# Performance work log

Measured on AMD Instinct MI355X. Metric: run time of the kernel, lower is better.

Reference implementation:

```python
import jax, jax.numpy as jnp
import numpy as np

R = 45        # num_dep_rels
L = 384       # sent_len
D = 512       # word representation dim = in_size*2
E_REL = 15    # dep_rel_emb_size
IN4 = 1024    # in_size*4
HOPS = 3
THRESH = 1e-06


def setup_inputs() -> dict:
    key = jax.random.key(0)
    ks = jax.random.split(key, 10)
    energy = jax.random.uniform(ks[0], (1, R, L, L), dtype=jnp.float32)
    word_h = jax.random.normal(ks[1], (1, L, D), dtype=jnp.float32)
    e1 = jax.random.normal(ks[2], (D,), dtype=jnp.float32)
    e2 = jax.random.normal(ks[3], (D,), dtype=jnp.float32)
    # learned params
    rel_embs = jax.random.normal(ks[4], (R, E_REL), dtype=jnp.float32)
    Wc = jax.random.normal(ks[5], (2 * D + E_REL, D), dtype=jnp.float32) * 0.02
    bc = jnp.zeros((D,), dtype=jnp.float32)
    Wk = jax.random.normal(ks[6], (HOPS, IN4, IN4), dtype=jnp.float32) * 0.02
    bk = jnp.zeros((HOPS, IN4), dtype=jnp.float32)
    Wh = jax.random.normal(ks[7], (HOPS, IN4, IN4), dtype=jnp.float32) * 0.02
    bh = jnp.zeros((HOPS, IN4), dtype=jnp.float32)
    return {"energy": energy, "word_h": word_h, "e1": e1, "e2": e2,
            "sent_len": L, "rel_embs": rel_embs, "Wc": Wc, "bc": bc,
            "Wk": Wk, "bk": bk, "Wh": Wh, "bh": bh}


def reference(energy, word_h, e1, e2, sent_len, rel_embs, Wc, bc, Wk, bk, Wh, bh):
    Ls = sent_len
    E = energy[0, :, :Ls, :Ls]                 # [R, L, L]
    marg = E.sum(axis=0)                       # [L, L] marginal energy
    # threshold back-off (try t, t/10, t/100 until some arc survives)
    m0 = marg > THRESH
    m1 = marg > THRESH * 0.1
    m2 = marg > THRESH * 0.01
    mask = jnp.where(m0.any(), m0, jnp.where(m1.any(), m1, m2))  # [L, L]

    H = word_h[0, :Ls]                         # [L, D]
    w = marg.reshape(-1)                       # [L*L] arc weights
    # rel embedding per arc: sum_r E[r,h,d] * rel_embs[r,e]
    rels = jnp.einsum('rhd,re->hde', E, rel_embs).reshape(Ls * Ls, E_REL)
    head_t = jnp.repeat(H, Ls, axis=0) * w[:, None]   # [L*L, D]
    dep_t = jnp.tile(H, (Ls, 1)) * w[:, None]         # [L*L, D]
    arc_in = jnp.concatenate([head_t, rels, dep_t], axis=1)  # [L*L, 2D+15]
    mem_bank = jax.nn.leaky_relu(arc_in @ Wc + bc)    # [L*L, D] (dropout=eval)
    maskf = mask.reshape(-1)                          # [L*L]

    # multi-hop memory attention; filtered-out arcs get zero attention weight
    inputs = jnp.concatenate([e1, e2])                # [1024]
    for i in range(HOPS):
        kv = inputs @ Wk[i] + bk[i]                   # [1024]
        k_, v_ = jnp.split(kv, 2)                     # chunk along dim 0
        k_ = jnp.tanh(k_)
        v_ = jax.nn.leaky_relu(v_)
        scores = jnp.where(maskf, mem_bank @ k_, -1e30)  # [L*L]
        dist = jax.nn.softmax(scores)
        mem_rep = dist @ mem_bank                     # [D]
        inputs = jax.nn.leaky_relu(jnp.concatenate([v_, mem_rep]) @ Wh[i] + bh[i])
    return inputs
```

## Files before the change

### kernel.cpp

```cpp
#include <hip/hip_runtime.h>
#include <hip/hip_bf16.h>
#include <cstdint>
#include <cstddef>

#define LL      147456
#define NBLK    768
#define CHB     12
#define NPACK   288

typedef __attribute__((ext_vector_type(8))) short  short8;
typedef __attribute__((ext_vector_type(4))) float  f32x4;

#define EPACK_OFF   0u
#define MARG_OFF    14155776u
#define A_OFF       14745600u
#define BT_OFF      15532032u
#define UTGP_OFF    16318464u
#define XIN_OFF     16367696u
#define KBUF_OFF    16371792u
#define VBUF_OFF    16373840u
#define PM_OFF      16379984u
#define PL_OFF      16383056u
#define PACC_OFF    16386128u
#define SRAW_OFF    17958992u
#define BLKF_OFF    18548816u

#define SKIP_LD     30.0f

static __device__ __forceinline__ ushort f2bf(float x) {
  uint u = __float_as_uint(x);
  return (ushort)((u + 0x7fffu + ((u >> 16) & 1u)) >> 16);
}
static __device__ __forceinline__ float lrelu(float x) { return fmaxf(x, 0.01f * x); }

__global__ __launch_bounds__(256) void k_prep(
    const float* __restrict__ E, uint4* __restrict__ ep,
    float* __restrict__ marg, int* __restrict__ blkflags,
    const float* __restrict__ H, const float* __restrict__ Wc,
    const float* __restrict__ rel, const float* __restrict__ bc,
    float* __restrict__ A, float* __restrict__ Btp, uint4* __restrict__ Utgp) {
  __shared__ float Hs[4][512];
  __shared__ float Ps[4][512];
  __shared__ int fsh;
  int b = blockIdx.x, t = threadIdx.x;
  if (b < 192) {
    bool roleA = (b < 96);
    int g0 = (roleA ? b : b - 96) * 4;
    const float* Wcp = Wc + (size_t)(roleA ? 0 : 527) * 512;
    float* dst = roleA ? A : Btp;
    for (int i = t; i < 4 * 512; i += 256) Hs[i >> 9][i & 511] = H[(size_t)g0 * 512 + i];
    __syncthreads();
    int cq = t & 127, q = t >> 7;
    int c0 = cq * 4;
    f32x4 acc[4];
#pragma unroll
    for (int i = 0; i < 4; ++i) acc[i] = (f32x4){0.f, 0.f, 0.f, 0.f};
    for (int k = q * 256; k < q * 256 + 256; ++k) {
      f32x4 wv = *(const f32x4*)&Wcp[(size_t)k * 512 + c0];
#pragma unroll
      for (int i = 0; i < 4; ++i) { float hv = Hs[i][k]; acc[i] += hv * wv; }
    }
    if (q == 1) {
#pragma unroll
      for (int i = 0; i < 4; ++i) *(f32x4*)&Ps[i][c0] = acc[i];
    }
    __syncthreads();
    if (q == 0) {
#pragma unroll
      for (int i = 0; i < 4; ++i) {
        acc[i] += *(const f32x4*)&Ps[i][c0];
        *(f32x4*)&dst[(size_t)(g0 + i) * 512 + c0] = acc[i];
      }
    }
  } else if (b == 192) {
    for (int c = t; c < 512; c += 256) {
      float uv[48];
#pragma unroll
      for (int k = 0; k < 45; ++k) {
        float s = 0.f;
#pragma unroll
        for (int e = 0; e < 15; ++e) s += rel[k * 15 + e] * Wc[(size_t)(512 + e) * 512 + c];
        uv[k] = s;
      }
      uv[45] = bc[c]; uv[46] = 0.f; uv[47] = 0.f;
#pragma unroll
      for (int g = 0; g < 6; ++g) {
        uint w[4];
#pragma unroll
        for (int p = 0; p < 4; ++p)
          w[p] = (uint)f2bf(uv[g * 8 + 2 * p]) | ((uint)f2bf(uv[g * 8 + 2 * p + 1]) << 16);
        uint4 v; v.x = w[0]; v.y = w[1]; v.z = w[2]; v.w = w[3];
        Utgp[g * 512 + c] = v;
      }
    }
  } else {
    if (t == 0) fsh = 0;
    int bp = b - 193;
    size_t hd0 = (size_t)bp * 512 + 2 * t;
    float2 ev[46];
#pragma unroll
    for (int r = 0; r < 45; ++r) ev[r] = *(const float2*)&E[(size_t)r * LL + hd0];
    ev[45] = make_float2(1.0f, 1.0f);
    float s0 = 0.f, s1 = 0.f;
#pragma unroll
    for (int r = 0; r < 45; ++r) { s0 += ev[r].x; s1 += ev[r].y; }
#pragma unroll
    for (int o = 0; o < 6; ++o) {
      uint wa[4], wb[4];
#pragma unroll
      for (int p = 0; p < 4; ++p) {
        int r0 = 8 * o + 2 * p, r1 = r0 + 1;
        float a0 = (r0 < 46) ? ev[r0].x : 0.f, a1 = (r1 < 46) ? ev[r1].x : 0.f;
        float b0 = (r0 < 46) ? ev[r0].y : 0.f, b1 = (r1 < 46) ? ev[r1].y : 0.f;
        wa[p] = (uint)f2bf(a0) | ((uint)f2bf(a1) << 16);
        wb[p] = (uint)f2bf(b0) | ((uint)f2bf(b1) << 16);
      }
      uint4 va; va.x = wa[0]; va.y = wa[1]; va.z = wa[2]; va.w = wa[3];
      uint4 vb; vb.x = wb[0]; vb.y = wb[1]; vb.z = wb[2]; vb.w = wb[3];
      ep[(size_t)o * LL + hd0] = va;
      ep[(size_t)o * LL + hd0 + 1] = vb;
    }
    *(float2*)&marg[hd0] = make_float2(s0, s1);
    int f = (s0 > 1e-6f ? 1 : 0) | (s0 > 1e-7f ? 2 : 0) | (s0 > 1e-8f ? 4 : 0)
          | (s1 > 1e-6f ? 1 : 0) | (s1 > 1e-7f ? 2 : 0) | (s1 > 1e-8f ? 4 : 0);
#pragma unroll
    for (int d = 1; d < 64; d <<= 1) f |= __shfl_xor(f, d);
    __syncthreads();
    if ((t & 63) == 0) atomicOr(&fsh, f);
    __syncthreads();
    if (t == 0) blkflags[bp] = fsh;
  }
}

__global__ __launch_bounds__(256) void k_gemv(const float* __restrict__ W, const float* __restrict__ bias,
                                              const float* __restrict__ xA, const float* __restrict__ xB,
                                              float* __restrict__ outA, float* __restrict__ outB) {
  __shared__ float xs[1024];
  __shared__ float red[8][32];
  int t = threadIdx.x;
  for (int i = t; i < 1024; i += 256) xs[i] = (i < 512) ? xA[i] : xB[i - 512];
  __syncthreads();
  int jj = t & 31, kq = t >> 5;
  int j = blockIdx.x * 32 + jj;
  float acc = 0.f;
#pragma unroll 8
  for (int k = kq * 128; k < kq * 128 + 128; ++k) acc = fmaf(xs[k], W[(size_t)k * 1024 + j], acc);
  red[kq][jj] = acc;
  __syncthreads();
  if (kq == 0) {
    float s = bias[j];
#pragma unroll
    for (int q = 0; q < 8; ++q) s += red[q][jj];
    if (j < 512) outA[j] = tanhf(s);
    else outB[j - 512] = lrelu(s);
  }
}

__global__ __launch_bounds__(256, 3) void k_scores(
    const uint4* __restrict__ ep, const float* __restrict__ marg,
    const float* __restrict__ A, const float* __restrict__ Btp,
    const uint4* __restrict__ Utgp, const int* __restrict__ blkflags,
    const float* __restrict__ kvec,
    float* __restrict__ pm, float* __restrict__ pl, float* __restrict__ sraw) {
  __shared__ __align__(16) uint4 uthF[6 * 512];
  __shared__ float sbuf[CHB * 16];
  __shared__ float redw[8];
  __shared__ int fsh;
  int t = threadIdx.x, b = blockIdx.x;
  int dbt = b >> 5, hg = b & 31;
  int dbase = dbt * 16, h0 = hg * CHB;
  int lane = t & 63, wid = t >> 6;
  int l15 = lane & 15, qq = lane >> 4;

  if (t == 0) fsh = 0;
  for (int i = t; i < 6 * 512; i += 256) uthF[i] = Utgp[i];
  int f = 0;
  for (int i = t; i < NPACK; i += 256) f |= blkflags[i];
#pragma unroll
  for (int d = 1; d < 64; d <<= 1) f |= __shfl_xor(f, d);

  const short8 zero8 = (short8){0, 0, 0, 0, 0, 0, 0, 0};
  short8 a0[3], a1[3];
  f32x4 wq[3];
#pragma unroll
  for (int k3 = 0; k3 < 3; ++k3) {
    int h = h0 + wid * 3 + k3;
    int hda = h * 384 + dbase + l15;
    uint4 r0 = ep[(size_t)qq * LL + hda];
    a0[k3] = *(short8*)&r0;
    if (qq < 2) { uint4 r1 = ep[(size_t)(4 + qq) * LL + hda]; a1[k3] = *(short8*)&r1; }
    else a1[k3] = zero8;
    wq[k3] = *(const f32x4*)&marg[h * 384 + dbase + qq * 4];
  }
  __syncthreads();
  if ((t & 63) == 0) atomicOr(&fsh, f);

  float sp[3][4];
#pragma unroll
  for (int k3 = 0; k3 < 3; ++k3)
#pragma unroll
    for (int j = 0; j < 4; ++j) sp[k3][j] = 0.f;

  for (int half = 0; half < 2; ++half) {
    float kreg[16];
#pragma unroll
    for (int tt = 0; tt < 16; ++tt) kreg[tt] = kvec[half * 256 + tt * 16 + l15];
#pragma unroll 4
    for (int tt = 0; tt < 16; ++tt) {
      int c = half * 256 + tt * 16 + l15;
      short8 b0 = *(short8*)&uthF[qq * 512 + c];
      short8 b1 = (qq < 2) ? *(short8*)&uthF[(4 + qq) * 512 + c] : zero8;
      const float* Bp = &Btp[(size_t)(dbase + qq * 4) * 512 + c];
      float bt0 = Bp[0], bt1 = Bp[512], bt2 = Bp[1024], bt3 = Bp[1536];
      const float* Ap = &A[(size_t)(h0 + wid * 3) * 512 + c];
      float av[3]; av[0] = Ap[0]; av[1] = Ap[512]; av[2] = Ap[1024];
#pragma unroll
      for (int k3 = 0; k3 < 3; ++k3) {
        f32x4 cc = (f32x4){0.f, 0.f, 0.f, 0.f};
        cc = __builtin_amdgcn_mfma_f32_16x16x32_bf16(a0[k3], b0, cc, 0, 0, 0);
        cc = __builtin_amdgcn_mfma_f32_16x16x32_bf16(a1[k3], b1, cc, 0, 0, 0);
        float aw = av[k3];
        float x0 = cc[0] + wq[k3][0] * (aw + bt0); float mb0 = fmaxf(x0, 0.01f * x0);
        float x1 = cc[1] + wq[k3][1] * (aw + bt1); float mb1 = fmaxf(x1, 0.01f * x1);
        float x2 = cc[2] + wq[k3][2] * (aw + bt2); float mb2 = fmaxf(x2, 0.01f * x2);
        float x3 = cc[3] + wq[k3][3] * (aw + bt3); float mb3 = fmaxf(x3, 0.01f * x3);
        sp[k3][0] = fmaf(mb0, kreg[tt], sp[k3][0]);
        sp[k3][1] = fmaf(mb1, kreg[tt], sp[k3][1]);
        sp[k3][2] = fmaf(mb2, kreg[tt], sp[k3][2]);
        sp[k3][3] = fmaf(mb3, kreg[tt], sp[k3][3]);
      }
    }
  }
#pragma unroll
  for (int k3 = 0; k3 < 3; ++k3)
#pragma unroll
    for (int j = 0; j < 4; ++j) {
#pragma unroll
      for (int d = 1; d < 16; d <<= 1) sp[k3][j] += __shfl_xor(sp[k3][j], d);
    }
  __syncthreads();
  float thr = (fsh & 1) ? 1e-6f : ((fsh & 2) ? 1e-7f : 1e-8f);
  if (l15 == 0) {
#pragma unroll
    for (int k3 = 0; k3 < 3; ++k3) {
      int base = (wid * 3 + k3) * 16 + qq * 4;
#pragma unroll
      for (int j = 0; j < 4; ++j)
        sbuf[base + j] = (wq[k3][j] > thr) ? sp[k3][j] : -1e30f;
    }
  }
  __syncthreads();
  float s = (t < CHB * 16) ? sbuf[t] : -1e30f;
  float m = s;
#pragma unroll
  for (int d = 1; d < 64; d <<= 1) m = fmaxf(m, __shfl_xor(m, d));
  if (lane == 0) redw[wid] = m;
  __syncthreads();
  float mloc = fmaxf(fmaxf(redw[0], redw[1]), fmaxf(redw[2], redw[3]));
  float e = (t < CHB * 16) ? __expf(s - mloc) : 0.f;
#pragma unroll
  for (int d = 1; d < 64; d <<= 1) e += __shfl_xor(e, d);
  if (lane == 0) redw[4 + wid] = e;
  if (t < CHB * 16) sraw[(size_t)b * 192 + t] = s;
  __syncthreads();
  if (t == 0) { pm[b] = mloc; pl[b] = redw[4] + redw[5] + redw[6] + redw[7]; }
}

__global__ __launch_bounds__(256, 3) void k_pv(
    const uint4* __restrict__ ep, const float* __restrict__ marg,
    const float* __restrict__ A, const float* __restrict__ Btp,
    const uint4* __restrict__ Utgp, const float* __restrict__ pm,
    const float* __restrict__ sraw, float* __restrict__ pacc) {
  __shared__ __align__(16) uint4 uthF[6 * 512];
  __shared__ float pbuf[CHB * 16];
  __shared__ float paccs[256];
  __shared__ float redm[4];
  int t = threadIdx.x, b = blockIdx.x;
  int lane = t & 63, wid = t >> 6;

  float m = -1e30f;
  for (int i = t; i < NBLK; i += 256) m = fmaxf(m, pm[i]);
#pragma unroll
  for (int d = 1; d < 64; d <<= 1) m = fmaxf(m, __shfl_xor(m, d));
  if (lane == 0) redm[wid] = m;
  __syncthreads();
  float M = fmaxf(fmaxf(redm[0], redm[1]), fmaxf(redm[2], redm[3]));
  float pmb = pm[b];
  if (pmb - M < -SKIP_LD) return;

  int dbt = b >> 5, hg = b & 31;
  int dbase = dbt * 16, h0 = hg * CHB;
  int l15 = lane & 15, qq = lane >> 4;

  for (int i = t; i < 6 * 512; i += 256) uthF[i] = Utgp[i];
  if (t < CHB * 16) pbuf[t] = __expf(sraw[(size_t)b * 192 + t] - pmb);

  const short8 zero8 = (short8){0, 0, 0, 0, 0, 0, 0, 0};
  short8 a0[3], a1[3];
  f32x4 wq[3];
#pragma unroll
  for (int k3 = 0; k3 < 3; ++k3) {
    int h = h0 + wid * 3 + k3;
    int hda = h * 384 + dbase + l15;
    uint4 r0 = ep[(size_t)qq * LL + hda];
    a0[k3] = *(short8*)&r0;
    if (qq < 2) { uint4 r1 = ep[(size_t)(4 + qq) * LL + hda]; a1[k3] = *(short8*)&r1; }
    else a1[k3] = zero8;
    wq[k3] = *(const f32x4*)&marg[h * 384 + dbase + qq * 4];
  }
  __syncthreads();

  float pvw[3][4];
#pragma unroll
  for (int k3 = 0; k3 < 3; ++k3)
#pragma unroll
    for (int j = 0; j < 4; ++j)
      pvw[k3][j] = pbuf[(wid * 3 + k3) * 16 + qq * 4 + j];

  for (int half = 0; half < 2; ++half) {
    paccs[t] = 0.f;
    __syncthreads();
#pragma unroll 4
    for (int tt = 0; tt < 16; ++tt) {
      int c = half * 256 + tt * 16 + l15;
      short8 b0 = *(short8*)&uthF[qq * 512 + c];
      short8 b1 = (qq < 2) ? *(short8*)&uthF[(4 + qq) * 512 + c] : zero8;
      const float* Bp = &Btp[(size_t)(dbase + qq * 4) * 512 + c];
      float bt0 = Bp[0], bt1 = Bp[512], bt2 = Bp[1024], bt3 = Bp[1536];
      const float* Ap = &A[(size_t)(h0 + wid * 3) * 512 + c];
      float av[3]; av[0] = Ap[0]; av[1] = Ap[512]; av[2] = Ap[1024];
      float acc_t = 0.f;
#pragma unroll
      for (int k3 = 0; k3 < 3; ++k3) {
        f32x4 cc = (f32x4){0.f, 0.f, 0.f, 0.f};
        cc = __builtin_amdgcn_mfma_f32_16x16x32_bf16(a0[k3], b0, cc, 0, 0, 0);
        cc = __builtin_amdgcn_mfma_f32_16x16x32_bf16(a1[k3], b1, cc, 0, 0, 0);
        float aw = av[k3];
        float x0 = cc[0] + wq[k3][0] * (aw + bt0); float mb0 = fmaxf(x0, 0.01f * x0);
        float x1 = cc[1] + wq[k3][1] * (aw + bt1); float mb1 = fmaxf(x1, 0.01f * x1);
        float x2 = cc[2] + wq[k3][2] * (aw + bt2); float mb2 = fmaxf(x2, 0.01f * x2);
        float x3 = cc[3] + wq[k3][3] * (aw + bt3); float mb3 = fmaxf(x3, 0.01f * x3);
        acc_t = fmaf(pvw[k3][0], mb0, fmaf(pvw[k3][1], mb1,
                fmaf(pvw[k3][2], mb2, fmaf(pvw[k3][3], mb3, acc_t))));
      }
      acc_t += __shfl_xor(acc_t, 16);
      acc_t += __shfl_xor(acc_t, 32);
      if (lane < 16) atomicAdd(&paccs[tt * 16 + l15], acc_t);
    }
    __syncthreads();
    pacc[(size_t)b * 512 + half * 256 + t] = paccs[t];
    __syncthreads();
  }
}

__global__ __launch_bounds__(256) void k_gemvc(
    const float* __restrict__ W, const float* __restrict__ bias,
    const float* __restrict__ vbuf, const float* __restrict__ pm,
    const float* __restrict__ pl, const float* __restrict__ pacc,
    float* __restrict__ outA, float* __restrict__ out2) {
  __shared__ float xs[1024];
  __shared__ float sc[NBLK];
  __shared__ int slist[NBLK];
  __shared__ int scnt_sh;
  __shared__ float redm[8];
  __shared__ float red[8][32];
  int t = threadIdx.x;
  int lane = t & 63, wid = t >> 6;

  float m = -1e30f;
  for (int i = t; i < NBLK; i += 256) m = fmaxf(m, pm[i]);
#pragma unroll
  for (int d = 1; d < 64; d <<= 1) m = fmaxf(m, __shfl_xor(m, d));
  if (lane == 0) redm[wid] = m;
  __syncthreads();
  float M = fmaxf(fmaxf(redm[0], redm[1]), fmaxf(redm[2], redm[3]));
  float ls = 0.f;
  for (int i = t; i < NBLK; i += 256) {
    float d = pm[i] - M;
    float e = (d < -SKIP_LD) ? 0.f : __expf(d);
    sc[i] = e;
    ls += e * pl[i];
  }
#pragma unroll
  for (int d = 1; d < 64; d <<= 1) ls += __shfl_xor(ls, d);
  if (lane == 0) redm[4 + wid] = ls;
  __syncthreads();
  float L = redm[4] + redm[5] + redm[6] + redm[7];

  if (wid == 0) {
    int cnt = 0;
#pragma unroll
    for (int rnd = 0; rnd < NBLK / 64; ++rnd) {
      int bb = rnd * 64 + lane;
      bool p = sc[bb] > 0.f;
      unsigned long long mask = __ballot(p);
      int off = __popcll(mask & ((1ull << lane) - 1ull));
      if (p) slist[cnt + off] = bb;
      cnt += __popcll(mask);
    }
    if (lane == 0) scnt_sh = cnt;
  }
  __syncthreads();
  int S = scnt_sh;
  for (int c = t; c < 512; c += 256) xs[c] = vbuf[c];
#pragma unroll
  for (int half = 0; half < 2; ++half) {
    int c = t + half * 256;
    float s = 0.f;
    for (int k = 0; k < S; ++k) {
      int bb = slist[k];
      s += pacc[(size_t)bb * 512 + c] * sc[bb];
    }
    xs[512 + c] = s / L;
  }
  __syncthreads();

  int jj = t & 31, kq = t >> 5;
  int j = blockIdx.x * 32 + jj;
  float acc = 0.f;
#pragma unroll 8
  for (int k = kq * 128; k < kq * 128 + 128; ++k) acc = fmaf(xs[k], W[(size_t)k * 1024 + j], acc);
  red[kq][jj] = acc;
  __syncthreads();
  if (kq == 0) {
    float s = bias[j];
#pragma unroll
    for (int q = 0; q < 8; ++q) s += red[q][jj];
    float rv = lrelu(s);
    outA[j] = rv;
    if (out2) out2[j] = rv;
  }
}

extern "C" void kernel_launch(void* const* d_in, const int* in_sizes, int n_in,
                              void* d_out, int out_size, void* d_ws, size_t ws_size,
                              hipStream_t stream) {
  const float* E   = (const float*)d_in[0];
  const float* H   = (const float*)d_in[1];
  const float* e1  = (const float*)d_in[2];
  const float* e2  = (const float*)d_in[3];
  const float* rel = (const float*)d_in[5];
  const float* Wc  = (const float*)d_in[6];
  const float* bc  = (const float*)d_in[7];
  const float* Wk  = (const float*)d_in[8];
  const float* bk  = (const float*)d_in[9];
  const float* Wh  = (const float*)d_in[10];
  const float* bh  = (const float*)d_in[11];

  char* ws = (char*)d_ws;
  uint4*  ep     = (uint4*)(ws + EPACK_OFF);
  float*  marg   = (float*)(ws + MARG_OFF);
  float*  Abuf   = (float*)(ws + A_OFF);
  float*  Btp    = (float*)(ws + BT_OFF);
  uint4*  Utgp   = (uint4*)(ws + UTGP_OFF);
  float*  xin    = (float*)(ws + XIN_OFF);
  float*  kbuf   = (float*)(ws + KBUF_OFF);
  float*  vbuf   = (float*)(ws + VBUF_OFF);
  float*  pm     = (float*)(ws + PM_OFF);
  float*  pl     = (float*)(ws + PL_OFF);
  float*  pacc   = (float*)(ws + PACC_OFF);
  float*  sraw   = (float*)(ws + SRAW_OFF);
  int*    blkf   = (int*)(ws + BLKF_OFF);

  k_prep<<<481, 256, 0, stream>>>(E, ep, marg, blkf, H, Wc, rel, bc, Abuf, Btp, Utgp);

  for (int hop = 0; hop < 3; ++hop) {
    const float* Wki = Wk + (size_t)hop * 1024 * 1024;
    const float* bki = bk + (size_t)hop * 1024;
    const float* Whi = Wh + (size_t)hop * 1024 * 1024;
    const float* bhi = bh + (size_t)hop * 1024;
    k_gemv<<<32, 256, 0, stream>>>(Wki, bki, hop == 0 ? e1 : xin,
                                   hop == 0 ? e2 : xin + 512, kbuf, vbuf);
    k_scores<<<NBLK, 256, 0, stream>>>(ep, marg, Abuf, Btp, Utgp, blkf, kbuf, pm, pl, sraw);
    k_pv<<<NBLK, 256, 0, stream>>>(ep, marg, Abuf, Btp, Utgp, pm, sraw, pacc);
    k_gemvc<<<32, 256, 0, stream>>>(Whi, bhi, vbuf, pm, pl, pacc, xin,
                                    hop == 2 ? (float*)d_out : (float*)nullptr);
  }
}
```

Before: 207.8 us.

## Fold softmax normalization into k_pv with atomic memrep and smaller head chunks

Each PV block now computes the global max and normalizer itself, scales its partial sum, and atomically adds it into a 512-wide memrep vector. This removes the per-block pacc buffer and the dedicated combine kernel, so k_gemv is reused for the output projection. Head chunking drops from 12 to 8 rows, giving 1152 blocks at 4 waves per SIMD. Btp is stored transposed so bias loads are single f32x4 reads, and the LDS staging of Utgp is dropped in favour of direct global loads. The changes add global atomics (making summation order nondeterministic), a redundant max/sum reduction in every block, and a tighter skip threshold.

```diff
diff --git a/kernel.cpp b/kernel.cpp
--- a/kernel.cpp
+++ b/kernel.cpp
@@ -4,8 +4,8 @@
 #include <cstddef>
 
 #define LL      147456
-#define NBLK    768
-#define CHB     12
+#define NBLK    1152
+#define CHB     8
 #define NPACK   288
 
 typedef __attribute__((ext_vector_type(8))) short  short8;
@@ -14,18 +14,18 @@
 #define EPACK_OFF   0u
 #define MARG_OFF    14155776u
 #define A_OFF       14745600u
-#define BT_OFF      15532032u
+#define BTC_OFF     15532032u
 #define UTGP_OFF    16318464u
-#define XIN_OFF     16367696u
-#define KBUF_OFF    16371792u
-#define VBUF_OFF    16373840u
-#define PM_OFF      16379984u
-#define PL_OFF      16383056u
-#define PACC_OFF    16386128u
-#define SRAW_OFF    17958992u
-#define BLKF_OFF    18548816u
-
-#define SKIP_LD     30.0f
+#define XIN_OFF     16367616u
+#define KBUF_OFF    16371712u
+#define VBUF_OFF    16373760u
+#define MEMREP_OFF  16375808u
+#define PM_OFF      16377856u
+#define PL_OFF      16382464u
+#define SRAW_OFF    16387072u
+#define BLKF_OFF    16976896u
+
+#define SKIP_LD     20.0f
 
 static __device__ __forceinline__ ushort f2bf(float x) {
   uint u = __float_as_uint(x);
@@ -38,7 +38,7 @@
     float* __restrict__ marg, int* __restrict__ blkflags,
     const float* __restrict__ H, const float* __restrict__ Wc,
     const float* __restrict__ rel, const float* __restrict__ bc,
-    float* __restrict__ A, float* __restrict__ Btp, uint4* __restrict__ Utgp) {
+    float* __restrict__ A, float* __restrict__ Btc, uint4* __restrict__ Utgp) {
   __shared__ float Hs[4][512];
   __shared__ float Ps[4][512];
   __shared__ int fsh;
@@ -47,7 +47,6 @@
     bool roleA = (b < 96);
     int g0 = (roleA ? b : b - 96) * 4;
     const float* Wcp = Wc + (size_t)(roleA ? 0 : 527) * 512;
-    float* dst = roleA ? A : Btp;
     for (int i = t; i < 4 * 512; i += 256) Hs[i >> 9][i & 511] = H[(size_t)g0 * 512 + i];
     __syncthreads();
     int cq = t & 127, q = t >> 7;
@@ -69,7 +68,12 @@
 #pragma unroll
       for (int i = 0; i < 4; ++i) {
         acc[i] += *(const f32x4*)&Ps[i][c0];
-        *(f32x4*)&dst[(size_t)(g0 + i) * 512 + c0] = acc[i];
+        if (roleA) {
+          *(f32x4*)&A[(size_t)(g0 + i) * 512 + c0] = acc[i];
+        } else {
+#pragma unroll
+          for (int j = 0; j < 4; ++j) Btc[(size_t)(c0 + j) * 384 + (g0 + i)] = acc[i][j];
+        }
       }
     }
   } else if (b == 192) {
@@ -134,7 +138,8 @@
 
 __global__ __launch_bounds__(256) void k_gemv(const float* __restrict__ W, const float* __restrict__ bias,
                                               const float* __restrict__ xA, const float* __restrict__ xB,
-                                              float* __restrict__ outA, float* __restrict__ outB) {
+                                              float* __restrict__ outA, float* __restrict__ outB,
+                                              float* __restrict__ out2, int mode) {
   __shared__ float xs[1024];
   __shared__ float red[8][32];
   int t = threadIdx.x;
@@ -151,40 +156,46 @@
     float s = bias[j];
 #pragma unroll
     for (int q = 0; q < 8; ++q) s += red[q][jj];
-    if (j < 512) outA[j] = tanhf(s);
-    else outB[j - 512] = lrelu(s);
-  }
-}
-
-__global__ __launch_bounds__(256, 3) void k_scores(
+    if (mode == 0) {
+      if (j < 512) outA[j] = tanhf(s);
+      else outB[j - 512] = lrelu(s);
+    } else {
+      float rv = lrelu(s);
+      outA[j] = rv;
+      if (out2) out2[j] = rv;
+    }
+  }
+}
+
+__global__ __launch_bounds__(256, 4) void k_scores(
     const uint4* __restrict__ ep, const float* __restrict__ marg,
-    const float* __restrict__ A, const float* __restrict__ Btp,
+    const float* __restrict__ A, const float* __restrict__ Btc,
     const uint4* __restrict__ Utgp, const int* __restrict__ blkflags,
     const float* __restrict__ kvec,
-    float* __restrict__ pm, float* __restrict__ pl, float* __restrict__ sraw) {
-  __shared__ __align__(16) uint4 uthF[6 * 512];
+    float* __restrict__ pm, float* __restrict__ pl, float* __restrict__ sraw,
+    float* __restrict__ memrep) {
   __shared__ float sbuf[CHB * 16];
   __shared__ float redw[8];
   __shared__ int fsh;
   int t = threadIdx.x, b = blockIdx.x;
-  int dbt = b >> 5, hg = b & 31;
+  int dbt = b / 48, hg = b - dbt * 48;
   int dbase = dbt * 16, h0 = hg * CHB;
   int lane = t & 63, wid = t >> 6;
   int l15 = lane & 15, qq = lane >> 4;
 
+  if (b == 0) { memrep[t] = 0.f; memrep[t + 256] = 0.f; }
   if (t == 0) fsh = 0;
-  for (int i = t; i < 6 * 512; i += 256) uthF[i] = Utgp[i];
   int f = 0;
   for (int i = t; i < NPACK; i += 256) f |= blkflags[i];
 #pragma unroll
   for (int d = 1; d < 64; d <<= 1) f |= __shfl_xor(f, d);
 
   const short8 zero8 = (short8){0, 0, 0, 0, 0, 0, 0, 0};
-  short8 a0[3], a1[3];
-  f32x4 wq[3];
-#pragma unroll
-  for (int k3 = 0; k3 < 3; ++k3) {
-    int h = h0 + wid * 3 + k3;
+  short8 a0[2], a1[2];
+  f32x4 wq[2];
+#pragma unroll
+  for (int k3 = 0; k3 < 2; ++k3) {
+    int h = h0 + wid * 2 + k3;
     int hda = h * 384 + dbase + l15;
     uint4 r0 = ep[(size_t)qq * LL + hda];
     a0[k3] = *(short8*)&r0;
@@ -195,9 +206,9 @@
   __syncthreads();
   if ((t & 63) == 0) atomicOr(&fsh, f);
 
-  float sp[3][4];
-#pragma unroll
-  for (int k3 = 0; k3 < 3; ++k3)
+  float sp[2][4];
+#pragma unroll
+  for (int k3 = 0; k3 < 2; ++k3)
 #pragma unroll
     for (int j = 0; j < 4; ++j) sp[k3][j] = 0.f;
 
@@ -208,22 +219,21 @@
 #pragma unroll 4
     for (int tt = 0; tt < 16; ++tt) {
       int c = half * 256 + tt * 16 + l15;
-      short8 b0 = *(short8*)&uthF[qq * 512 + c];
-      short8 b1 = (qq < 2) ? *(short8*)&uthF[(4 + qq) * 512 + c] : zero8;
-      const float* Bp = &Btp[(size_t)(dbase + qq * 4) * 512 + c];
-      float bt0 = Bp[0], bt1 = Bp[512], bt2 = Bp[1024], bt3 = Bp[1536];
-      const float* Ap = &A[(size_t)(h0 + wid * 3) * 512 + c];
-      float av[3]; av[0] = Ap[0]; av[1] = Ap[512]; av[2] = Ap[1024];
-#pragma unroll
-      for (int k3 = 0; k3 < 3; ++k3) {
+      short8 b0 = *(const short8*)&Utgp[qq * 512 + c];
+      short8 b1 = (qq < 2) ? *(const short8*)&Utgp[(4 + qq) * 512 + c] : zero8;
+      f32x4 btv = *(const f32x4*)&Btc[(size_t)c * 384 + dbase + qq * 4];
+      const float* Ap = &A[(size_t)(h0 + wid * 2) * 512 + c];
+      float av[2]; av[0] = Ap[0]; av[1] = Ap[512];
+#pragma unroll
+      for (int k3 = 0; k3 < 2; ++k3) {
         f32x4 cc = (f32x4){0.f, 0.f, 0.f, 0.f};
         cc = __builtin_amdgcn_mfma_f32_16x16x32_bf16(a0[k3], b0, cc, 0, 0, 0);
         cc = __builtin_amdgcn_mfma_f32_16x16x32_bf16(a1[k3], b1, cc, 0, 0, 0);
         float aw = av[k3];
-        float x0 = cc[0] + wq[k3][0] * (aw + bt0); float mb0 = fmaxf(x0, 0.01f * x0);
-        float x1 = cc[1] + wq[k3][1] * (aw + bt1); float mb1 = fmaxf(x1, 0.01f * x1);
-        float x2 = cc[2] + wq[k3][2] * (aw + bt2); float mb2 = fmaxf(x2, 0.01f * x2);
-        float x3 = cc[3] + wq[k3][3] * (aw + bt3); float mb3 = fmaxf(x3, 0.01f * x3);
+        float x0 = cc[0] + wq[k3][0] * (aw + btv[0]); float mb0 = fmaxf(x0, 0.01f * x0);
+        float x1 = cc[1] + wq[k3][1] * (aw + btv[1]); float mb1 = fmaxf(x1, 0.01f * x1);
+        float x2 = cc[2] + wq[k3][2] * (aw + btv[2]); float mb2 = fmaxf(x2, 0.01f * x2);
+        float x3 = cc[3] + wq[k3][3] * (aw + btv[3]); float mb3 = fmaxf(x3, 0.01f * x3);
         sp[k3][0] = fmaf(mb0, kreg[tt], sp[k3][0]);
         sp[k3][1] = fmaf(mb1, kreg[tt], sp[k3][1]);
         sp[k3][2] = fmaf(mb2, kreg[tt], sp[k3][2]);
@@ -232,7 +242,7 @@
     }
   }
 #pragma unroll
-  for (int k3 = 0; k3 < 3; ++k3)
+  for (int k3 = 0; k3 < 2; ++k3)
 #pragma unroll
     for (int j = 0; j < 4; ++j) {
 #pragma unroll
@@ -242,8 +252,8 @@
   float thr = (fsh & 1) ? 1e-6f : ((fsh & 2) ? 1e-7f : 1e-8f);
   if (l15 == 0) {
 #pragma unroll
-    for (int k3 = 0; k3 < 3; ++k3) {
-      int base = (wid * 3 + k3) * 16 + qq * 4;
+    for (int k3 = 0; k3 < 2; ++k3) {
+      int base = (wid * 2 + k3) * 16 + qq * 4;
 #pragma unroll
       for (int j = 0; j < 4; ++j)
         sbuf[base + j] = (wq[k3][j] > thr) ? sp[k3][j] : -1e30f;
@@ -261,20 +271,20 @@
 #pragma unroll
   for (int d = 1; d < 64; d <<= 1) e += __shfl_xor(e, d);
   if (lane == 0) redw[4 + wid] = e;
-  if (t < CHB * 16) sraw[(size_t)b * 192 + t] = s;
+  if (t < CHB * 16) sraw[(size_t)b * 128 + t] = s;
   __syncthreads();
   if (t == 0) { pm[b] = mloc; pl[b] = redw[4] + redw[5] + redw[6] + redw[7]; }
 }
 
-__global__ __launch_bounds__(256, 3) void k_pv(
+__global__ __launch_bounds__(256, 4) void k_pv(
     const uint4* __restrict__ ep, const float* __restrict__ marg,
-    const float* __restrict__ A, const float* __restrict__ Btp,
+    const float* __restrict__ A, const float* __restrict__ Btc,
     const uint4* __restrict__ Utgp, const float* __restrict__ pm,
-    const float* __restrict__ sraw, float* __restrict__ pacc) {
-  __shared__ __align__(16) uint4 uthF[6 * 512];
+    const float* __restrict__ pl, const float* __restrict__ sraw,
+    float* __restrict__ memrep) {
   __shared__ float pbuf[CHB * 16];
   __shared__ float paccs[256];
-  __shared__ float redm[4];
+  __shared__ float redm[8];
   int t = threadIdx.x, b = blockIdx.x;
   int lane = t & 63, wid = t >> 6;
 
@@ -285,22 +295,32 @@
   if (lane == 0) redm[wid] = m;
   __syncthreads();
   float M = fmaxf(fmaxf(redm[0], redm[1]), fmaxf(redm[2], redm[3]));
+  float ls = 0.f;
+  for (int i = t; i < NBLK; i += 256) {
+    float d = pm[i] - M;
+    if (!(d < -SKIP_LD)) ls += __expf(d) * pl[i];
+  }
+#pragma unroll
+  for (int d = 1; d < 64; d <<= 1) ls += __shfl_xor(ls, d);
+  if (lane == 0) redm[4 + wid] = ls;
+  __syncthreads();
+  float L = redm[4] + redm[5] + redm[6] + redm[7];
   float pmb = pm[b];
   if (pmb - M < -SKIP_LD) return;
-
-  int dbt = b >> 5, hg = b & 31;
+  float w = __expf(pmb - M) / L;
+
+  int dbt = b / 48, hg = b - dbt * 48;
   int dbase = dbt * 16, h0 = hg * CHB;
   int l15 = lane & 15, qq = lane >> 4;
 
-  for (int i = t; i < 6 * 512; i += 256) uthF[i] = Utgp[i];
-  if (t < CHB * 16) pbuf[t] = __expf(sraw[(size_t)b * 192 + t] - pmb);
+  if (t < CHB * 16) pbuf[t] = __expf(sraw[(size_t)b * 128 + t] - pmb);
 
   const short8 zero8 = (short8){0, 0, 0, 0, 0, 0, 0, 0};
-  short8 a0[3], a1[3];
-  f32x4 wq[3];
-#pragma unroll
-  for (int k3 = 0; k3 < 3; ++k3) {
-    int h = h0 + wid * 3 + k3;
+  short8 a0[2], a1[2];
+  f32x4 wq[2];
+#pragma unroll
+  for (int k3 = 0; k3 < 2; ++k3) {
+    int h = h0 + wid * 2 + k3;
     int hda = h * 384 + dbase + l15;
     uint4 r0 = ep[(size_t)qq * LL + hda];
     a0[k3] = *(short8*)&r0;
@@ -310,12 +330,12 @@
   }
   __syncthreads();
 
-  float pvw[3][4];
-#pragma unroll
-  for (int k3 = 0; k3 < 3; ++k3)
+  float pvw[2][4];
+#pragma unroll
+  for (int k3 = 0; k3 < 2; ++k3)
 #pragma unroll
     for (int j = 0; j < 4; ++j)
-      pvw[k3][j] = pbuf[(wid * 3 + k3) * 16 + qq * 4 + j];
+      pvw[k3][j] = pbuf[(wid * 2 + k3) * 16 + qq * 4 + j];
 
   for (int half = 0; half < 2; ++half) {
     paccs[t] = 0.f;
@@ -323,23 +343,22 @@
 #pragma unroll 4
     for (int tt = 0; tt < 16; ++tt) {
       int c = half * 256 + tt * 16 + l15;
-      short8 b0 = *(short8*)&uthF[qq * 512 + c];
-      short8 b1 = (qq < 2) ? *(short8*)&uthF[(4 + qq) * 512 + c] : zero8;
-      const float* Bp = &Btp[(size_t)(dbase + qq * 4) * 512 + c];
-      float bt0 = Bp[0], bt1 = Bp[512], bt2 = Bp[1024], bt3 = Bp[1536];
-      const float* Ap = &A[(size_t)(h0 + wid * 3) * 512 + c];
-      float av[3]; av[0] = Ap[0]; av[1] = Ap[512]; av[2] = Ap[1024];
+      short8 b0 = *(const short8*)&Utgp[qq * 512 + c];
+      short8 b1 = (qq < 2) ? *(const short8*)&Utgp[(4 + qq) * 512 + c] : zero8;
+      f32x4 btv = *(const f32x4*)&Btc[(size_t)c * 384 + dbase + qq * 4];
+      const float* Ap = &A[(size_t)(h0 + wid * 2) * 512 + c];
+      float av[2]; av[0] = Ap[0]; av[1] = Ap[512];
       float acc_t = 0.f;
 #pragma unroll
-      for (int k3 = 0; k3 < 3; ++k3) {
+      for (int k3 = 0; k3 < 2; ++k3) {
         f32x4 cc = (f32x4){0.f, 0.f, 0.f, 0.f};
         cc = __builtin_amdgcn_mfma_f32_16x16x32_bf16(a0[k3], b0, cc, 0, 0, 0);
         cc = __builtin_amdgcn_mfma_f32_16x16x32_bf16(a1[k3], b1, cc, 0, 0, 0);
         float aw = av[k3];
-        float x0 = cc[0] + wq[k3][0] * (aw + bt0); float mb0 = fmaxf(x0, 0.01f * x0);
-        float x1 = cc[1] + wq[k3][1] * (aw + bt1); float mb1 = fmaxf(x1, 0.01f * x1);
-        float x2 = cc[2] + wq[k3][2] * (aw + bt2); float mb2 = fmaxf(x2, 0.01f * x2);
-        float x3 = cc[3] + wq[k3][3] * (aw + bt3); float mb3 = fmaxf(x3, 0.01f * x3);
+        float x0 = cc[0] + wq[k3][0] * (aw + btv[0]); float mb0 = fmaxf(x0, 0.01f * x0);
+        float x1 = cc[1] + wq[k3][1] * (aw + btv[1]); float mb1 = fmaxf(x1, 0.01f * x1);
+        float x2 = cc[2] + wq[k3][2] * (aw + btv[2]); float mb2 = fmaxf(x2, 0.01f * x2);
+        float x3 = cc[3] + wq[k3][3] * (aw + btv[3]); float mb3 = fmaxf(x3, 0.01f * x3);
         acc_t = fmaf(pvw[k3][0], mb0, fmaf(pvw[k3][1], mb1,
                 fmaf(pvw[k3][2], mb2, fmaf(pvw[k3][3], mb3, acc_t))));
       }
@@ -348,87 +367,8 @@
       if (lane < 16) atomicAdd(&paccs[tt * 16 + l15], acc_t);
     }
     __syncthreads();
-    pacc[(size_t)b * 512 + half * 256 + t] = paccs[t];
-    __syncthreads();
-  }
-}
-
-__global__ __launch_bounds__(256) void k_gemvc(
-    const float* __restrict__ W, const float* __restrict__ bias,
-    const float* __restrict__ vbuf, const float* __restrict__ pm,
-    const float* __restrict__ pl, const float* __restrict__ pacc,
-    float* __restrict__ outA, float* __restrict__ out2) {
-  __shared__ float xs[1024];
-  __shared__ float sc[NBLK];
-  __shared__ int slist[NBLK];
-  __shared__ int scnt_sh;
-  __shared__ float redm[8];
-  __shared__ float red[8][32];
-  int t = threadIdx.x;
-  int lane = t & 63, wid = t >> 6;
-
-  float m = -1e30f;
-  for (int i = t; i < NBLK; i += 256) m = fmaxf(m, pm[i]);
-#pragma unroll
-  for (int d = 1; d < 64; d <<= 1) m = fmaxf(m, __shfl_xor(m, d));
-  if (lane == 0) redm[wid] = m;
-  __syncthreads();
-  float M = fmaxf(fmaxf(redm[0], redm[1]), fmaxf(redm[2], redm[3]));
-  float ls = 0.f;
-  for (int i = t; i < NBLK; i += 256) {
-    float d = pm[i] - M;
-    float e = (d < -SKIP_LD) ? 0.f : __expf(d);
-    sc[i] = e;
-    ls += e * pl[i];
-  }
-#pragma unroll
-  for (int d = 1; d < 64; d <<= 1) ls += __shfl_xor(ls, d);
-  if (lane == 0) redm[4 + wid] = ls;
-  __syncthreads();
-  float L = redm[4] + redm[5] + redm[6] + redm[7];
-
-  if (wid == 0) {
-    int cnt = 0;
-#pragma unroll
-    for (int rnd = 0; rnd < NBLK / 64; ++rnd) {
-      int bb = rnd * 64 + lane;
-      bool p = sc[bb] > 0.f;
-      unsigned long long mask = __ballot(p);
-      int off = __popcll(mask & ((1ull << lane) - 1ull));
-      if (p) slist[cnt + off] = bb;
-      cnt += __popcll(mask);
-    }
-    if (lane == 0) scnt_sh = cnt;
-  }
-  __syncthreads();
-  int S = scnt_sh;
-  for (int c = t; c < 512; c += 256) xs[c] = vbuf[c];
-#pragma unroll
-  for (int half = 0; half < 2; ++half) {
-    int c = t + half * 256;
-    float s = 0.f;
-    for (int k = 0; k < S; ++k) {
-      int bb = slist[k];
-      s += pacc[(size_t)bb * 512 + c] * sc[bb];
-    }
-    xs[512 + c] = s / L;
-  }
-  __syncthreads();
-
-  int jj = t & 31, kq = t >> 5;
-  int j = blockIdx.x * 32 + jj;
-  float acc = 0.f;
-#pragma unroll 8
-  for (int k = kq * 128; k < kq * 128 + 128; ++k) acc = fmaf(xs[k], W[(size_t)k * 1024 + j], acc);
-  red[kq][jj] = acc;
-  __syncthreads();
-  if (kq == 0) {
-    float s = bias[j];
-#pragma unroll
-    for (int q = 0; q < 8; ++q) s += red[q][jj];
-    float rv = lrelu(s);
-    outA[j] = rv;
-    if (out2) out2[j] = rv;
+    atomicAdd(&memrep[half * 256 + t], paccs[t] * w);
+    __syncthreads();
   }
 }
 
@@ -451,18 +391,18 @@
   uint4*  ep     = (uint4*)(ws + EPACK_OFF);
   float*  marg   = (float*)(ws + MARG_OFF);
   float*  Abuf   = (float*)(ws + A_OFF);
-  float*  Btp    = (float*)(ws + BT_OFF);
+  float*  Btc    = (float*)(ws + BTC_OFF);
   uint4*  Utgp   = (uint4*)(ws + UTGP_OFF);
   float*  xin    = (float*)(ws + XIN_OFF);
   float*  kbuf   = (float*)(ws + KBUF_OFF);
   float*  vbuf   = (float*)(ws + VBUF_OFF);
+  float*  memrep = (float*)(ws + MEMREP_OFF);
   float*  pm     = (float*)(ws + PM_OFF);
   float*  pl     = (float*)(ws + PL_OFF);
-  float*  pacc   = (float*)(ws + PACC_OFF);
   float*  sraw   = (float*)(ws + SRAW_OFF);
   int*    blkf   = (int*)(ws + BLKF_OFF);
 
-  k_prep<<<481, 256, 0, stream>>>(E, ep, marg, blkf, H, Wc, rel, bc, Abuf, Btp, Utgp);
+  k_prep<<<481, 256, 0, stream>>>(E, ep, marg, blkf, H, Wc, rel, bc, Abuf, Btc, Utgp);
 
   for (int hop = 0; hop < 3; ++hop) {
     const float* Wki = Wk + (size_t)hop * 1024 * 1024;
@@ -470,10 +410,12 @@
     const float* Whi = Wh + (size_t)hop * 1024 * 1024;
     const float* bhi = bh + (size_t)hop * 1024;
     k_gemv<<<32, 256, 0, stream>>>(Wki, bki, hop == 0 ? e1 : xin,
-                                   hop == 0 ? e2 : xin + 512, kbuf, vbuf);
-    k_scores<<<NBLK, 256, 0, stream>>>(ep, marg, Abuf, Btp, Utgp, blkf, kbuf, pm, pl, sraw);
-    k_pv<<<NBLK, 256, 0, stream>>>(ep, marg, Abuf, Btp, Utgp, pm, sraw, pacc);
-    k_gemvc<<<32, 256, 0, stream>>>(Whi, bhi, vbuf, pm, pl, pacc, xin,
-                                    hop == 2 ? (float*)d_out : (float*)nullptr);
-  }
-}
+                                   hop == 0 ? e2 : xin + 512, kbuf, vbuf,
+                                   (float*)nullptr, 0);
+    k_scores<<<NBLK, 256, 0, stream>>>(ep, marg, Abuf, Btc, Utgp, blkf, kbuf,
+                                       pm, pl, sraw, memrep);
+    k_pv<<<NBLK, 256, 0, stream>>>(ep, marg, Abuf, Btc, Utgp, pm, pl, sraw, memrep);
+    k_gemv<<<32, 256, 0, stream>>>(Whi, bhi, vbuf, memrep, xin, (float*)nullptr,
+                                   hop == 2 ? (float*)d_out : (float*)nullptr, 1);
+  }
+}
```

Result: slower. 257.0 us (+23.7%).
